# Kernel optimization log

Hardware: AMD Instinct MI355X
Metric: run time of the kernel (lower is better)

Reference implementation:

```python
import jax, jax.numpy as jnp
import numpy as np

N_HEAD = 12

def setup_inputs() -> dict:
    key = jax.random.key(0)
    k1, k2, k3 = jax.random.split(key, 3)
    B, T, C = 8, 1024, 768
    x = jax.random.normal(k1, (B, T, C), dtype=jnp.float32)
    # Linear weights stored as [in, out] so y = x @ W + b (same math as torch Linear)
    w_attn = jax.random.normal(k2, (C, 3 * C), dtype=jnp.float32) * (1.0 / np.sqrt(C))
    b_attn = jnp.zeros((3 * C,), dtype=jnp.float32)
    w_proj = jax.random.normal(k3, (C, C), dtype=jnp.float32) * (1.0 / np.sqrt(C))
    b_proj = jnp.zeros((C,), dtype=jnp.float32)
    return {"x": x, "w_attn": w_attn, "b_attn": b_attn, "w_proj": w_proj, "b_proj": b_proj}

def reference(x, w_attn, b_attn, w_proj, b_proj):
    B, T, C = x.shape
    H = N_HEAD
    D = C // H
    qkv = x @ w_attn + b_attn                        # [B,T,3C]
    q, k, v = jnp.split(qkv, 3, axis=-1)             # each [B,T,C]
    q = q.reshape(B, T, H, D).transpose(0, 2, 1, 3)  # [B,H,T,D]
    k = k.reshape(B, T, H, D).transpose(0, 2, 1, 3)
    v = v.reshape(B, T, H, D).transpose(0, 2, 1, 3)
    scale = 1.0 / jnp.sqrt(jnp.asarray(D, dtype=x.dtype))
    att = jnp.einsum('bhqd,bhkd->bhqk', q, k) * scale  # [B,H,T,T]
    causal = jnp.tril(jnp.ones((T, T), dtype=bool))    # [T,T]
    att = jnp.where(causal[None, None], att, jnp.asarray(-jnp.inf, dtype=att.dtype))
    att = jax.nn.softmax(att, axis=-1)
    out = jnp.einsum('bhqk,bhkd->bhqd', att, v)        # [B,H,T,D]
    out = out.transpose(0, 2, 1, 3).reshape(B, T, C)
    return out @ w_proj + b_proj
```

## Files before the change

### kernel.cpp

```cpp
#include <hip/hip_runtime.h>
#include <hip/hip_bf16.h>
#include <cmath>

#define B_ 8
#define T_ 1024
#define C_ 768
#define H_ 12
#define D_ 64
#define N3C 2304
#define M_ 8192

typedef __bf16 bf16x4 __attribute__((ext_vector_type(4)));
typedef __bf16 bf16x8 __attribute__((ext_vector_type(8)));
typedef float  f32x4  __attribute__((ext_vector_type(4)));

typedef const __attribute__((address_space(1))) void* gptr_t;
typedef __attribute__((address_space(3))) void* lptr_t;

#define LOG2E 1.44269504088896f

__device__ __forceinline__ bf16x8 cvt_bf16x8(const float4& a, const float4& b) {
    bf16x8 r;
    r[0] = (__bf16)a.x; r[1] = (__bf16)a.y; r[2] = (__bf16)a.z; r[3] = (__bf16)a.w;
    r[4] = (__bf16)b.x; r[5] = (__bf16)b.y; r[6] = (__bf16)b.z; r[7] = (__bf16)b.w;
    return r;
}

__global__ __launch_bounds__(256) void prepass(const float* __restrict__ x,
                                               __bf16* __restrict__ xb,
                                               const float* __restrict__ wa,
                                               __bf16* __restrict__ wat,
                                               const float* __restrict__ wp,
                                               __bf16* __restrict__ wpt) {
    __shared__ float tile[32][33];
    const int bx = blockIdx.x, tid = threadIdx.x;
    if (bx < 3072) {
        int i = (bx * 256 + tid) * 8;
        float4 a = *(const float4*)&x[i];
        float4 b = *(const float4*)&x[i + 4];
        *(bf16x8*)&xb[i] = cvt_bf16x8(a, b);
        return;
    }
    const float* w;
    __bf16* wt;
    int K, N, n0, k0;
    if (bx < 4800) {
        int bb = bx - 3072;
        w = wa; wt = wat; K = 768; N = 2304;
        n0 = (bb % 72) * 32; k0 = (bb / 72) * 32;
    } else {
        int bb = bx - 4800;
        w = wp; wt = wpt; K = 768; N = 768;
        n0 = (bb % 24) * 32; k0 = (bb / 24) * 32;
    }
    int tx = tid & 31, ty = tid >> 5;
#pragma unroll
    for (int i = 0; i < 4; i++)
        tile[ty + i * 8][tx] = w[(size_t)(k0 + ty + i * 8) * N + n0 + tx];
    __syncthreads();
#pragma unroll
    for (int i = 0; i < 4; i++)
        wt[(size_t)(n0 + ty + i * 8) * K + k0 + tx] = (__bf16)tile[tx][ty + i * 8];
}

__global__ __launch_bounds__(256) void qkv_gemm_mfma(const __bf16* __restrict__ A,
                                                     const __bf16* __restrict__ Bt,
                                                     const float* __restrict__ bias,
                                                     __bf16* __restrict__ qb,
                                                     __bf16* __restrict__ kb,
                                                     __bf16* __restrict__ vbt) {
    __shared__ __bf16 smem[2][2][128 * 64];
    const int tid = threadIdx.x;
    const int wave = tid >> 6, lane = tid & 63;
    const int lane15 = lane & 15, quad = lane >> 4;
    const int bid = blockIdx.x;
    const int m0 = ((bid & 7) * 8 + ((bid >> 3) & 7)) * 128;
    const int n0 = (bid >> 6) * 128;
    const int wm = (wave >> 1) * 64, wn = (wave & 1) * 64;
    f32x4 acc[4][4] = {};

#define QSTAGE(KC, BUF)                                                             \
    {                                                                               \
        const int k0s = (KC) * 64;                                                  \
        _Pragma("unroll")                                                           \
        for (int r = 0; r < 4; ++r) {                                               \
            int p = r * 256 + tid;                                                  \
            int mrow = p >> 3, csw = p & 7;                                         \
            int ksrc = (csw ^ (mrow & 7)) * 8;                                      \
            __builtin_amdgcn_global_load_lds(                                       \
                (gptr_t)(A + (size_t)(m0 + mrow) * 768 + k0s + ksrc),               \
                (lptr_t)(&smem[BUF][0][0] + (r * 256 + wave * 64) * 8), 16, 0, 0);  \
            __builtin_amdgcn_global_load_lds(                                       \
                (gptr_t)(Bt + (size_t)(n0 + mrow) * 768 + k0s + ksrc),              \
                (lptr_t)(&smem[BUF][1][0] + (r * 256 + wave * 64) * 8), 16, 0, 0);  \
        }                                                                           \
    }

    QSTAGE(0, 0);
    for (int kc = 0; kc < 12; ++kc) {
        __syncthreads();
        if (kc + 1 < 12) QSTAGE(kc + 1, (kc + 1) & 1);
        const __bf16* As = &smem[kc & 1][0][0];
        const __bf16* Bs = &smem[kc & 1][1][0];
#pragma unroll
        for (int ks = 0; ks < 2; ++ks) {
            bf16x8 af[4], bf[4];
#pragma unroll
            for (int mt = 0; mt < 4; ++mt) {
                int m = wm + mt * 16 + lane15;
                int csw = (ks * 4 + quad) ^ (m & 7);
                af[mt] = *(const bf16x8*)(As + m * 64 + csw * 8);
            }
#pragma unroll
            for (int nt = 0; nt < 4; ++nt) {
                int n = wn + nt * 16 + lane15;
                int csw = (ks * 4 + quad) ^ (n & 7);
                bf[nt] = *(const bf16x8*)(Bs + n * 64 + csw * 8);
            }
#pragma unroll
            for (int mt = 0; mt < 4; ++mt)
#pragma unroll
                for (int nt = 0; nt < 4; ++nt)
                    acc[mt][nt] = __builtin_amdgcn_mfma_f32_16x16x32_bf16(af[mt], bf[nt], acc[mt][nt], 0, 0, 0);
        }
    }
    __syncthreads();

    if (n0 < 1536) {
        const bool isq = (n0 < 768);
        const float sc = isq ? (0.125f * LOG2E) : 1.0f;
#pragma unroll
        for (int nt = 0; nt < 4; ++nt) {
            int n = n0 + wn + nt * 16 + lane15;
            int rem = isq ? n : (n - 768);
            int h = rem >> 6;
            int d = n & 63;
            float bv = bias[n];
            __bf16* dst = isq ? qb : kb;
#pragma unroll
            for (int mt = 0; mt < 4; ++mt) {
#pragma unroll
                for (int reg = 0; reg < 4; ++reg) {
                    int mr = m0 + wm + mt * 16 + quad * 4 + reg;
                    int bb = mr >> 10, t = mr & 1023;
                    dst[(((size_t)bb * H_ + h) * T_ + t) * D_ + d] =
                        (__bf16)((acc[mt][nt][reg] + bv) * sc);
                }
            }
        }
    } else {
        __bf16* vls = &smem[0][0][0];
#pragma unroll
        for (int nt = 0; nt < 4; ++nt) {
            int nl = wn + nt * 16 + lane15;
            float bv = bias[n0 + nl];
#pragma unroll
            for (int mt = 0; mt < 4; ++mt)
#pragma unroll
                for (int reg = 0; reg < 4; ++reg)
                    vls[nl * 136 + wm + mt * 16 + quad * 4 + reg] =
                        (__bf16)(acc[mt][nt][reg] + bv);
        }
        __syncthreads();
        int nl = tid >> 1;
        int t0 = (tid & 1) * 64;
        int n = n0 + nl;
        int h = (n - 1536) >> 6;
        int d = n & 63;
        int bb = m0 >> 10, tg = (m0 & 1023) + t0;
        __bf16* dst = vbt + (((size_t)bb * H_ + h) * D_ + d) * T_ + tg;
        const __bf16* srcl = vls + nl * 136 + t0;
#pragma unroll
        for (int c = 0; c < 8; ++c) {
            bf16x8 v;
#pragma unroll
            for (int i = 0; i < 8; ++i) {
                int s = c * 8 + i;
                v[i] = srcl[(s & 3) * 16 + (s >> 2)];
            }
            *(bf16x8*)(dst + c * 8) = v;
        }
    }
}

__global__ __launch_bounds__(256) void proj_gemm_mfma(const __bf16* __restrict__ A,
                                                      const __bf16* __restrict__ Bt,
                                                      const float* __restrict__ bias,
                                                      float* __restrict__ out) {
    __shared__ __bf16 As[2][128 * 64];
    __shared__ __bf16 Bs[2][64 * 64];
    const int tid = threadIdx.x;
    const int wave = tid >> 6, lane = tid & 63;
    const int lane15 = lane & 15, quad = lane >> 4;
    const int bid = blockIdx.x;
    const int m0 = ((bid & 7) * 8 + ((bid >> 3) & 7)) * 128;
    const int n0 = (bid >> 6) * 64;
    const int wm = wave * 32;
    f32x4 acc[2][4] = {};

#define PSTAGE(KC, BUF)                                                             \
    {                                                                               \
        const int k0s = (KC) * 64;                                                  \
        _Pragma("unroll")                                                           \
        for (int r = 0; r < 4; ++r) {                                               \
            int p = r * 256 + tid;                                                  \
            int mrow = p >> 3, csw = p & 7;                                         \
            int ksrc = (csw ^ (mrow & 7)) * 8;                                      \
            __builtin_amdgcn_global_load_lds(                                       \
                (gptr_t)(A + (size_t)(m0 + mrow) * 768 + k0s + ksrc),               \
                (lptr_t)(&As[BUF][0] + (r * 256 + wave * 64) * 8), 16, 0, 0);       \
        }                                                                           \
        _Pragma("unroll")                                                           \
        for (int r = 0; r < 2; ++r) {                                               \
            int p = r * 256 + tid;                                                  \
            int nrow = p >> 3, csw = p & 7;                                         \
            int ksrc = (csw ^ (nrow & 7)) * 8;                                      \
            __builtin_amdgcn_global_load_lds(                                       \
                (gptr_t)(Bt + (size_t)(n0 + nrow) * 768 + k0s + ksrc),              \
                (lptr_t)(&Bs[BUF][0] + (r * 256 + wave * 64) * 8), 16, 0, 0);       \
        }                                                                           \
    }

    PSTAGE(0, 0);
    for (int kc = 0; kc < 12; ++kc) {
        __syncthreads();
        if (kc + 1 < 12) PSTAGE(kc + 1, (kc + 1) & 1);
        const __bf16* Ac = &As[kc & 1][0];
        const __bf16* Bc = &Bs[kc & 1][0];
#pragma unroll
        for (int ks = 0; ks < 2; ++ks) {
            bf16x8 af[2], bf[4];
#pragma unroll
            for (int mt = 0; mt < 2; ++mt) {
                int m = wm + mt * 16 + lane15;
                int csw = (ks * 4 + quad) ^ (m & 7);
                af[mt] = *(const bf16x8*)(Ac + m * 64 + csw * 8);
            }
#pragma unroll
            for (int nt = 0; nt < 4; ++nt) {
                int n = nt * 16 + lane15;
                int csw = (ks * 4 + quad) ^ (n & 7);
                bf[nt] = *(const bf16x8*)(Bc + n * 64 + csw * 8);
            }
#pragma unroll
            for (int mt = 0; mt < 2; ++mt)
#pragma unroll
                for (int nt = 0; nt < 4; ++nt)
                    acc[mt][nt] = __builtin_amdgcn_mfma_f32_16x16x32_bf16(af[mt], bf[nt], acc[mt][nt], 0, 0, 0);
        }
    }

#pragma unroll
    for (int nt = 0; nt < 4; ++nt) {
        int n = n0 + nt * 16 + lane15;
        float bv = bias[n];
#pragma unroll
        for (int mt = 0; mt < 2; ++mt) {
#pragma unroll
            for (int reg = 0; reg < 4; ++reg) {
                int mr = m0 + wm + mt * 16 + quad * 4 + reg;
                out[(size_t)mr * C_ + n] = acc[mt][nt][reg] + bv;
            }
        }
    }
}

__global__ __launch_bounds__(256) void attn_mfma(const __bf16* __restrict__ qb,
                                                 const __bf16* __restrict__ kb,
                                                 const __bf16* __restrict__ vbt,
                                                 __bf16* __restrict__ ao) {
    __shared__ __bf16 Ks[2][64 * 64];
    __shared__ __bf16 Vts[2][64 * 64];
    __shared__ __bf16 Ps[4 * 32 * 72];

    const int tid = threadIdx.x;
    const int wave = tid >> 6, lane = tid & 63;
    const int lane15 = lane & 15, quad = lane >> 4;
    const int bh = blockIdx.x;
    const int qt = 7 - blockIdx.y;
    const int b = bh / H_, h = bh % H_;
    const int q0 = qt * 128;

    const __bf16* Kb = kb + (size_t)bh * T_ * D_;
    const __bf16* Vb = vbt + (size_t)bh * D_ * T_;
    __bf16* Pw = Ps + wave * 32 * 72;

    bf16x8 qf[2][2];
#pragma unroll
    for (int g = 0; g < 2; ++g) {
        const __bf16* qrow = qb + ((size_t)bh * T_ + q0 + wave * 32 + g * 16 + lane15) * D_ + quad * 8;
        qf[g][0] = *(const bf16x8*)qrow;
        qf[g][1] = *(const bf16x8*)(qrow + 32);
    }

    f32x4 o[2][4] = {};
    float lsum[2][4] = {};

    const int kunits = 2 * qt + 2;

#define ASTAGE(KU, BUF)                                                            \
    {                                                                              \
        const int k0s = (KU) * 64;                                                 \
        _Pragma("unroll")                                                          \
        for (int r = 0; r < 2; ++r) {                                              \
            int p = r * 256 + tid;                                                 \
            int row = p >> 3, c = p & 7;                                           \
            int cs = (c ^ (row & 7)) * 8;                                          \
            __builtin_amdgcn_global_load_lds(                                      \
                (gptr_t)(Kb + (size_t)(k0s + row) * D_ + cs),                      \
                (lptr_t)(&Ks[BUF][0] + (r * 256 + wave * 64) * 8), 16, 0, 0);      \
            __builtin_amdgcn_global_load_lds(                                      \
                (gptr_t)(Vb + (size_t)row * T_ + k0s + cs),                        \
                (lptr_t)(&Vts[BUF][0] + (r * 256 + wave * 64) * 8), 16, 0, 0);     \
        }                                                                          \
    }

    ASTAGE(0, 0);

    for (int ku = 0; ku < kunits; ++ku) {
        __syncthreads();
        if (ku + 1 < kunits) ASTAGE(ku + 1, (ku + 1) & 1);
        const __bf16* Kc = &Ks[ku & 1][0];
        const __bf16* Vc = &Vts[ku & 1][0];
        const int k0 = ku * 64;

        f32x4 s[2][4];
#pragma unroll
        for (int kt = 0; kt < 4; ++kt) {
            int row = kt * 16 + lane15;
            bf16x8 kf0 = *(const bf16x8*)(Kc + row * 64 + ((quad) ^ (row & 7)) * 8);
            bf16x8 kf1 = *(const bf16x8*)(Kc + row * 64 + ((4 + quad) ^ (row & 7)) * 8);
#pragma unroll
            for (int g = 0; g < 2; ++g) {
                f32x4 t = {};
                t = __builtin_amdgcn_mfma_f32_16x16x32_bf16(qf[g][0], kf0, t, 0, 0, 0);
                t = __builtin_amdgcn_mfma_f32_16x16x32_bf16(qf[g][1], kf1, t, 0, 0, 0);
                s[g][kt] = t;
            }
        }

        const bool diag = (ku >= 2 * qt);
#pragma unroll
        for (int g = 0; g < 2; ++g) {
#pragma unroll
            for (int r = 0; r < 4; ++r) {
                bf16x4 pk;
#pragma unroll
                for (int kt = 0; kt < 4; ++kt) {
                    int col = k0 + kt * 16 + lane15;
                    float p = __builtin_amdgcn_exp2f(s[g][kt][r]);
                    if (diag) {
                        int qrow = q0 + wave * 32 + g * 16 + quad * 4 + r;
                        if (col > qrow) p = 0.f;
                    }
                    lsum[g][r] += p;
                    pk[kt] = (__bf16)p;
                }
                *(bf16x4*)(Pw + (g * 16 + quad * 4 + r) * 72 + lane15 * 4) = pk;
            }
        }

        bf16x8 vf[4][2];
#pragma unroll
        for (int dt = 0; dt < 4; ++dt) {
            int row = dt * 16 + lane15;
#pragma unroll
            for (int half = 0; half < 2; ++half)
                vf[dt][half] = *(const bf16x8*)(Vc + row * 64 + ((half * 4 + quad) ^ (row & 7)) * 8);
        }
#pragma unroll
        for (int g = 0; g < 2; ++g) {
#pragma unroll
            for (int half = 0; half < 2; ++half) {
                bf16x8 pf = *(const bf16x8*)(Pw + (g * 16 + lane15) * 72 + half * 32 + quad * 8);
#pragma unroll
                for (int dt = 0; dt < 4; ++dt)
                    o[g][dt] = __builtin_amdgcn_mfma_f32_16x16x32_bf16(pf, vf[dt][half], o[g][dt], 0, 0, 0);
            }
        }
    }

#pragma unroll
    for (int g = 0; g < 2; ++g) {
        float inv[4];
#pragma unroll
        for (int r = 0; r < 4; ++r) {
            float ls = lsum[g][r];
            ls += __shfl_xor(ls, 1);
            ls += __shfl_xor(ls, 2);
            ls += __shfl_xor(ls, 4);
            ls += __shfl_xor(ls, 8);
            inv[r] = 1.0f / ls;
        }
#pragma unroll
        for (int dt = 0; dt < 4; ++dt) {
#pragma unroll
            for (int r = 0; r < 4; ++r) {
                int t = q0 + wave * 32 + g * 16 + quad * 4 + r;
                ao[((size_t)(b * T_ + t)) * C_ + h * 64 + dt * 16 + lane15] =
                    (__bf16)(o[g][dt][r] * inv[r]);
            }
        }
    }
}

extern "C" void kernel_launch(void* const* d_in, const int* in_sizes, int n_in,
                              void* d_out, int out_size, void* d_ws, size_t ws_size,
                              hipStream_t stream) {
    const float* x = (const float*)d_in[0];
    const float* w_attn = (const float*)d_in[1];
    const float* b_attn = (const float*)d_in[2];
    const float* w_proj = (const float*)d_in[3];
    const float* b_proj = (const float*)d_in[4];
    float* out = (float*)d_out;

    __bf16* xb = (__bf16*)d_ws;
    __bf16* wat = xb + (size_t)M_ * C_;
    __bf16* wpt = wat + (size_t)N3C * C_;
    __bf16* qb = wpt + (size_t)C_ * C_;
    __bf16* kb = qb + (size_t)96 * T_ * D_;
    __bf16* vbt = kb + (size_t)96 * T_ * D_;
    __bf16* ao = vbt + (size_t)96 * T_ * D_;

    prepass<<<5376, 256, 0, stream>>>(x, xb, w_attn, wat, w_proj, wpt);
    qkv_gemm_mfma<<<1152, 256, 0, stream>>>(xb, wat, b_attn, qb, kb, vbt);
    attn_mfma<<<dim3(96, 8), 256, 0, stream>>>(qb, kb, vbt, ao);
    proj_gemm_mfma<<<768, 256, 0, stream>>>(ao, wpt, b_proj, out);
}
```

Measured before the change: 172.6 us.

## Replace double-buffered LDS staging with single buffer in QKV and proj GEMMs

Both GEMM kernels drop their double-buffered shared-memory tiles and use one buffer, loading each K chunk and then computing on it with two barriers per iteration. This halves LDS use, about 34KB for QKV and 24KB for proj, which could let more blocks fit on each CU. The cost is that the global-to-LDS load for the next chunk no longer overlaps the MFMA work on the current one.

Measured after the change: 182.7 us. 1.06x slower.

```diff
diff --git a/kernel.cpp b/kernel.cpp
--- a/kernel.cpp
+++ b/kernel.cpp
@@ -69,7 +69,9 @@
                                                      __bf16* __restrict__ qb,
                                                      __bf16* __restrict__ kb,
                                                      __bf16* __restrict__ vbt) {
-    __shared__ __bf16 smem[2][2][128 * 64];
+    __shared__ __bf16 smem[128 * 136];
+    __bf16* As = smem;
+    __bf16* Bs = smem + 8192;
     const int tid = threadIdx.x;
     const int wave = tid >> 6, lane = tid & 63;
     const int lane15 = lane & 15, quad = lane >> 4;
@@ -79,7 +81,7 @@
     const int wm = (wave >> 1) * 64, wn = (wave & 1) * 64;
     f32x4 acc[4][4] = {};
 
-#define QSTAGE(KC, BUF)                                                             \
+#define QSTAGE(KC)                                                                  \
     {                                                                               \
         const int k0s = (KC) * 64;                                                  \
         _Pragma("unroll")                                                           \
@@ -89,19 +91,16 @@
             int ksrc = (csw ^ (mrow & 7)) * 8;                                      \
             __builtin_amdgcn_global_load_lds(                                       \
                 (gptr_t)(A + (size_t)(m0 + mrow) * 768 + k0s + ksrc),               \
-                (lptr_t)(&smem[BUF][0][0] + (r * 256 + wave * 64) * 8), 16, 0, 0);  \
+                (lptr_t)(As + (r * 256 + wave * 64) * 8), 16, 0, 0);                \
             __builtin_amdgcn_global_load_lds(                                       \
                 (gptr_t)(Bt + (size_t)(n0 + mrow) * 768 + k0s + ksrc),              \
-                (lptr_t)(&smem[BUF][1][0] + (r * 256 + wave * 64) * 8), 16, 0, 0);  \
+                (lptr_t)(Bs + (r * 256 + wave * 64) * 8), 16, 0, 0);                \
         }                                                                           \
     }
 
-    QSTAGE(0, 0);
     for (int kc = 0; kc < 12; ++kc) {
-        __syncthreads();
-        if (kc + 1 < 12) QSTAGE(kc + 1, (kc + 1) & 1);
-        const __bf16* As = &smem[kc & 1][0][0];
-        const __bf16* Bs = &smem[kc & 1][1][0];
+        QSTAGE(kc);
+        __syncthreads();
 #pragma unroll
         for (int ks = 0; ks < 2; ++ks) {
             bf16x8 af[4], bf[4];
@@ -123,8 +122,8 @@
                 for (int nt = 0; nt < 4; ++nt)
                     acc[mt][nt] = __builtin_amdgcn_mfma_f32_16x16x32_bf16(af[mt], bf[nt], acc[mt][nt], 0, 0, 0);
         }
-    }
-    __syncthreads();
+        __syncthreads();
+    }
 
     if (n0 < 1536) {
         const bool isq = (n0 < 768);
@@ -149,7 +148,7 @@
             }
         }
     } else {
-        __bf16* vls = &smem[0][0][0];
+        __bf16* vls = smem;
 #pragma unroll
         for (int nt = 0; nt < 4; ++nt) {
             int nl = wn + nt * 16 + lane15;
@@ -187,8 +186,8 @@
                                                       const __bf16* __restrict__ Bt,
                                                       const float* __restrict__ bias,
                                                       float* __restrict__ out) {
-    __shared__ __bf16 As[2][128 * 64];
-    __shared__ __bf16 Bs[2][64 * 64];
+    __shared__ __bf16 As[128 * 64];
+    __shared__ __bf16 Bs[64 * 64];
     const int tid = threadIdx.x;
     const int wave = tid >> 6, lane = tid & 63;
     const int lane15 = lane & 15, quad = lane >> 4;
@@ -198,7 +197,7 @@
     const int wm = wave * 32;
     f32x4 acc[2][4] = {};
 
-#define PSTAGE(KC, BUF)                                                             \
+#define PSTAGE(KC)                                                                  \
     {                                                                               \
         const int k0s = (KC) * 64;                                                  \
         _Pragma("unroll")                                                           \
@@ -208,7 +207,7 @@
             int ksrc = (csw ^ (mrow & 7)) * 8;                                      \
             __builtin_amdgcn_global_load_lds(                                       \
                 (gptr_t)(A + (size_t)(m0 + mrow) * 768 + k0s + ksrc),               \
-                (lptr_t)(&As[BUF][0] + (r * 256 + wave * 64) * 8), 16, 0, 0);       \
+                (lptr_t)(&As[0] + (r * 256 + wave * 64) * 8), 16, 0, 0);            \
         }                                                                           \
         _Pragma("unroll")                                                           \
         for (int r = 0; r < 2; ++r) {                                               \
@@ -217,16 +216,13 @@
             int ksrc = (csw ^ (nrow & 7)) * 8;                                      \
             __builtin_amdgcn_global_load_lds(                                       \
                 (gptr_t)(Bt + (size_t)(n0 + nrow) * 768 + k0s + ksrc),              \
-                (lptr_t)(&Bs[BUF][0] + (r * 256 + wave * 64) * 8), 16, 0, 0);       \
+                (lptr_t)(&Bs[0] + (r * 256 + wave * 64) * 8), 16, 0, 0);            \
         }                                                                           \
     }
 
-    PSTAGE(0, 0);
     for (int kc = 0; kc < 12; ++kc) {
-        __syncthreads();
-        if (kc + 1 < 12) PSTAGE(kc + 1, (kc + 1) & 1);
-        const __bf16* Ac = &As[kc & 1][0];
-        const __bf16* Bc = &Bs[kc & 1][0];
+        PSTAGE(kc);
+        __syncthreads();
 #pragma unroll
         for (int ks = 0; ks < 2; ++ks) {
             bf16x8 af[2], bf[4];
@@ -234,13 +230,13 @@
             for (int mt = 0; mt < 2; ++mt) {
                 int m = wm + mt * 16 + lane15;
                 int csw = (ks * 4 + quad) ^ (m & 7);
-                af[mt] = *(const bf16x8*)(Ac + m * 64 + csw * 8);
+                af[mt] = *(const bf16x8*)(&As[0] + m * 64 + csw * 8);
             }
 #pragma unroll
             for (int nt = 0; nt < 4; ++nt) {
                 int n = nt * 16 + lane15;
                 int csw = (ks * 4 + quad) ^ (n & 7);
-                bf[nt] = *(const bf16x8*)(Bc + n * 64 + csw * 8);
+                bf[nt] = *(const bf16x8*)(&Bs[0] + n * 64 + csw * 8);
             }
 #pragma unroll
             for (int mt = 0; mt < 2; ++mt)
@@ -248,6 +244,7 @@
                 for (int nt = 0; nt < 4; ++nt)
                     acc[mt][nt] = __builtin_amdgcn_mfma_f32_16x16x32_bf16(af[mt], bf[nt], acc[mt][nt], 0, 0, 0);
         }
+        __syncthreads();
     }
 
 #pragma unroll
```
